# Kernel optimization log

Measured on AMD Instinct MI355X. Metric: run time of the kernel, lower is better.

The kernel has to match this reference:

```python
import jax, jax.numpy as jnp
import numpy as np

T = 4096
I = 512    # input_size
H = 2048   # hidden_layer_size
O = 1      # output_size

def setup_inputs() -> dict:
    key = jax.random.key(0)
    ks = jax.random.split(key, 7)
    s_ih = 1.0 / np.sqrt(H)
    return {
        "input_seq": jax.random.normal(ks[0], (T, I), dtype=jnp.float32),
        "W_ih": jax.random.uniform(ks[1], (4 * H, I), minval=-s_ih, maxval=s_ih, dtype=jnp.float32),
        "W_hh": jax.random.uniform(ks[2], (4 * H, H), minval=-s_ih, maxval=s_ih, dtype=jnp.float32),
        "b_ih": jax.random.uniform(ks[3], (4 * H,), minval=-s_ih, maxval=s_ih, dtype=jnp.float32),
        "b_hh": jax.random.uniform(ks[4], (4 * H,), minval=-s_ih, maxval=s_ih, dtype=jnp.float32),
        "W_lin": jax.random.uniform(ks[5], (O, H), minval=-s_ih, maxval=s_ih, dtype=jnp.float32),
        "b_lin": jax.random.uniform(ks[6], (O,), minval=-s_ih, maxval=s_ih, dtype=jnp.float32),
    }

def _lstm_last_h(x, W_ih, W_hh, b_ih, b_hh):
    # Precompute input contributions for all timesteps: [T, 4H]
    x_gates = x @ W_ih.T + (b_ih + b_hh)
    h0 = jnp.zeros((H,), dtype=x.dtype)
    c0 = jnp.zeros((H,), dtype=x.dtype)

    def step(carry, xg):
        h, c = carry
        gates = xg + h @ W_hh.T  # [4H]
        i, f, g, o = jnp.split(gates, 4)  # PyTorch gate order: i, f, g, o
        i = jax.nn.sigmoid(i)
        f = jax.nn.sigmoid(f)
        g = jnp.tanh(g)
        o = jax.nn.sigmoid(o)
        c = f * c + i * g
        h = o * jnp.tanh(c)
        return (h, c), None

    (h_T, _), _ = jax.lax.scan(step, (h0, c0), x_gates)
    return h_T

def reference(input_seq, W_ih, W_hh, b_ih, b_hh, W_lin, b_lin):
    # Module returns predictions[-1] = linear(lstm_out[-1]); only last h is needed.
    h_T = _lstm_last_h(input_seq, W_ih, W_hh, b_ih, b_hh)
    return h_T @ W_lin.T + b_lin  # shape [O]
```

## Files before the change

### kernel.cpp

```cpp
#include <hip/hip_runtime.h>


#define T_STEPS 4096
#define HID     2048
#define GATES   8192
#define KIN     512
#define NWG     256
#define NTHR    512
#define NREP    4
#define XG_BYTES ((size_t)T_STEPS * GATES * 4)
#define HCOM_BYTES ((size_t)NREP * 2 * HID * 8)

typedef float v2f __attribute__((ext_vector_type(2)));

__device__ __forceinline__ float u2f(unsigned int u) {
    union { unsigned int u; float f; } x; x.u = u; return x.f;
}
__device__ __forceinline__ float fast_sigmoid(float x) {
    return 1.f / (1.f + __expf(-x));
}
__device__ __forceinline__ float fast_tanh(float x) {
    return 2.f / (1.f + __expf(-2.f * x)) - 1.f;
}

__global__ __launch_bounds__(256) void gemm_xg(const float* __restrict__ A,
                                               const float* __restrict__ B,
                                               const float* __restrict__ bih,
                                               const float* __restrict__ bhh,
                                               float* __restrict__ C) {
    __shared__ float As[32][68];
    __shared__ float Bs[32][68];
    const int t  = threadIdx.x;
    const int tx = t & 15, ty = t >> 4;
    const int m0 = blockIdx.y * 64, n0 = blockIdx.x * 64;
    const int sr = t >> 3, sc = (t & 7) * 4;

    float c[4][4] = {};
    for (int k0 = 0; k0 < KIN; k0 += 32) {
        float4 a0 = *(const float4*)(A + (size_t)(m0 + sr)      * KIN + k0 + sc);
        float4 a1 = *(const float4*)(A + (size_t)(m0 + sr + 32) * KIN + k0 + sc);
        float4 b0 = *(const float4*)(B + (size_t)(n0 + sr)      * KIN + k0 + sc);
        float4 b1 = *(const float4*)(B + (size_t)(n0 + sr + 32) * KIN + k0 + sc);
        __syncthreads();
        As[sc+0][sr] = a0.x; As[sc+1][sr] = a0.y; As[sc+2][sr] = a0.z; As[sc+3][sr] = a0.w;
        As[sc+0][sr+32] = a1.x; As[sc+1][sr+32] = a1.y; As[sc+2][sr+32] = a1.z; As[sc+3][sr+32] = a1.w;
        Bs[sc+0][sr] = b0.x; Bs[sc+1][sr] = b0.y; Bs[sc+2][sr] = b0.z; Bs[sc+3][sr] = b0.w;
        Bs[sc+0][sr+32] = b1.x; Bs[sc+1][sr+32] = b1.y; Bs[sc+2][sr+32] = b1.z; Bs[sc+3][sr+32] = b1.w;
        __syncthreads();
#pragma unroll
        for (int kk = 0; kk < 32; ++kk) {
            float4 av = *(const float4*)&As[kk][ty * 4];
            float4 bv = *(const float4*)&Bs[kk][tx * 4];
            c[0][0] = fmaf(av.x, bv.x, c[0][0]); c[0][1] = fmaf(av.x, bv.y, c[0][1]);
            c[0][2] = fmaf(av.x, bv.z, c[0][2]); c[0][3] = fmaf(av.x, bv.w, c[0][3]);
            c[1][0] = fmaf(av.y, bv.x, c[1][0]); c[1][1] = fmaf(av.y, bv.y, c[1][1]);
            c[1][2] = fmaf(av.y, bv.z, c[1][2]); c[1][3] = fmaf(av.y, bv.w, c[1][3]);
            c[2][0] = fmaf(av.z, bv.x, c[2][0]); c[2][1] = fmaf(av.z, bv.y, c[2][1]);
            c[2][2] = fmaf(av.z, bv.z, c[2][2]); c[2][3] = fmaf(av.z, bv.w, c[2][3]);
            c[3][0] = fmaf(av.w, bv.x, c[3][0]); c[3][1] = fmaf(av.w, bv.y, c[3][1]);
            c[3][2] = fmaf(av.w, bv.z, c[3][2]); c[3][3] = fmaf(av.w, bv.w, c[3][3]);
        }
    }
    const int col = n0 + tx * 4;
    float4 bias;
    bias.x = bih[col]   + bhh[col];
    bias.y = bih[col+1] + bhh[col+1];
    bias.z = bih[col+2] + bhh[col+2];
    bias.w = bih[col+3] + bhh[col+3];
#pragma unroll
    for (int i = 0; i < 4; ++i) {
        float4 o;
        o.x = c[i][0] + bias.x; o.y = c[i][1] + bias.y;
        o.z = c[i][2] + bias.z; o.w = c[i][3] + bias.w;
        *(float4*)(C + (size_t)(m0 + ty * 4 + i) * GATES + col) = o;
    }
}

template<int USE_XG>
__global__ __launch_bounds__(NTHR, 2) void lstm_rec(
    const float* __restrict__ X,
    const float* __restrict__ Wih,
    const float* __restrict__ xg,
    const float* __restrict__ Whh,
    const float* __restrict__ bih,
    const float* __restrict__ bhh,
    unsigned long long* __restrict__ hcom)
{
    const int t  = threadIdx.x;
    const int kc = t & 127;
    const int rg = t >> 7;
    const int j0 = blockIdx.x * 8;
    const int rep = blockIdx.x & (NREP - 1);

    v2f whh2[8][8];
#pragma unroll
    for (int m = 0; m < 8; ++m) {
        const float* wr = Whh + (size_t)(rg * HID + j0 + m) * HID + kc;
#pragma unroll
        for (int j = 0; j < 8; ++j) {
            v2f p; p.x = wr[(2 * j) * 128]; p.y = wr[(2 * j + 1) * 128];
            whh2[m][j] = p;
        }
    }
    float wih[8][4];
    if (!USE_XG) {
#pragma unroll
        for (int m = 0; m < 8; ++m) {
            float4 vx = *(const float4*)(Wih + (size_t)(rg * HID + j0 + m) * KIN + kc * 4);
            wih[m][0] = vx.x; wih[m][1] = vx.y; wih[m][2] = vx.z; wih[m][3] = vx.w;
        }
    }

    float brow = 0.f;
    if (t < 32) {
        const int grow = (t >> 3) * HID + j0 + (t & 7);
        brow = bih[grow] + bhh[grow];
    }

    __shared__ float hshare[HID];
    __shared__ float part[32 * 132];
    float c_state = 0.f;

    for (int s = 0; s < T_STEPS; ++s) {
        float xgv = 0.f;
        if (USE_XG && t < 32)
            xgv = xg[(size_t)s * GATES + (t >> 3) * HID + j0 + (t & 7)];

        v2f hv2[8];
        if (t < 128) {
            if (t >= 64 && s > 0) __builtin_amdgcn_s_sleep(8);
            const unsigned long long* hp = hcom + ((size_t)rep * 2 + (s & 1)) * HID;
            unsigned long long v[16];
            int guard = 1 << 18;
            for (;;) {
#pragma unroll
                for (int g = 0; g < 16; ++g)
                    v[g] = __hip_atomic_load(hp + g * 128 + kc, __ATOMIC_RELAXED,
                                             __HIP_MEMORY_SCOPE_AGENT);
                bool ok = true;
#pragma unroll
                for (int g = 0; g < 16; ++g)
                    ok &= ((unsigned int)v[g] >= (unsigned int)s);
                if (ok || --guard <= 0) break;
                __builtin_amdgcn_s_sleep(1);
            }
#pragma unroll
            for (int j = 0; j < 8; ++j) {
                v2f p;
                p.x = u2f((unsigned int)(v[2 * j] >> 32));
                p.y = u2f((unsigned int)(v[2 * j + 1] >> 32));
                hv2[j] = p;
                hshare[(2 * j) * 128 + kc]     = p.x;
                hshare[(2 * j + 1) * 128 + kc] = p.y;
            }
        }
        __syncthreads();
        if (t >= 128) {
#pragma unroll
            for (int j = 0; j < 8; ++j) {
                v2f p;
                p.x = hshare[(2 * j) * 128 + kc];
                p.y = hshare[(2 * j + 1) * 128 + kc];
                hv2[j] = p;
            }
        }

        v2f acc2[8];
        if (!USE_XG) {
            float4 x4 = *(const float4*)(X + (size_t)s * KIN + kc * 4);
#pragma unroll
            for (int m = 0; m < 8; ++m) {
                float a = wih[m][0] * x4.x;
                a = fmaf(wih[m][1], x4.y, a);
                a = fmaf(wih[m][2], x4.z, a);
                a = fmaf(wih[m][3], x4.w, a);
                v2f z; z.x = a; z.y = 0.f; acc2[m] = z;
            }
        } else {
#pragma unroll
            for (int m = 0; m < 8; ++m) { v2f z; z.x = 0.f; z.y = 0.f; acc2[m] = z; }
        }

#pragma unroll
        for (int m = 0; m < 8; ++m) {
            v2f a = acc2[m];
#pragma unroll
            for (int j = 0; j < 8; ++j)
                a = __builtin_elementwise_fma(whh2[m][j], hv2[j], a);
            acc2[m] = a;
        }
#pragma unroll
        for (int m = 0; m < 8; ++m)
            part[(rg * 8 + m) * 132 + kc] = acc2[m].x + acc2[m].y;
        __syncthreads();

        if (t < 64) {
            const int row = t & 31, half = t >> 5;
            const float4* p4 = (const float4*)(part + row * 132 + half * 64);
            float s0 = 0.f, s1 = 0.f, s2 = 0.f, s3 = 0.f;
#pragma unroll
            for (int i = 0; i < 16; ++i) {
                float4 pv = p4[i];
                s0 += pv.x; s1 += pv.y; s2 += pv.z; s3 += pv.w;
            }
            float sum = (s0 + s1) + (s2 + s3);
            sum += __shfl_xor(sum, 32, 64);
            sum += brow + xgv;
            const float a1 = __shfl_down(sum, 8, 64);
            const float a2 = __shfl_down(sum, 16, 64);
            const float a3 = __shfl_down(sum, 24, 64);
            if (t < 8) {
                const float i_s = fast_sigmoid(sum);
                const float f_s = fast_sigmoid(a1);
                const float g_t = fast_tanh(a2);
                const float o_s = fast_sigmoid(a3);
                c_state = f_s * c_state + i_s * g_t;
                const float h = o_s * fast_tanh(c_state);
                const unsigned long long pk =
                    ((unsigned long long)__float_as_uint(h) << 32) | (unsigned int)(s + 1);
                const size_t slot = (size_t)((s + 1) & 1) * HID + j0 + t;
#pragma unroll
                for (int r = 0; r < NREP; ++r)
                    __hip_atomic_store(&hcom[(size_t)r * 2 * HID + slot], pk,
                                       __ATOMIC_RELAXED, __HIP_MEMORY_SCOPE_AGENT);
            }
        }
    }
}

__global__ __launch_bounds__(256) void final_linear(const unsigned long long* __restrict__ hcom,
                                                    const float* __restrict__ Wlin,
                                                    const float* __restrict__ blin,
                                                    float* __restrict__ out) {
    __shared__ float red[4];
    const int t = threadIdx.x;
    float a = 0.f;
#pragma unroll
    for (int e = 0; e < 8; ++e) {
        const int idx = t * 8 + e;
        a = fmaf(Wlin[idx], u2f((unsigned int)(hcom[idx] >> 32)), a);
    }
#pragma unroll
    for (int m = 1; m < 64; m <<= 1) a += __shfl_xor(a, m, 64);
    if ((t & 63) == 0) red[t >> 6] = a;
    __syncthreads();
    if (t == 0) out[0] = red[0] + red[1] + red[2] + red[3] + blin[0];
}

extern "C" void kernel_launch(void* const* d_in, const int* in_sizes, int n_in,
                              void* d_out, int out_size, void* d_ws, size_t ws_size,
                              hipStream_t stream) {
    const float* X    = (const float*)d_in[0];
    const float* Wih  = (const float*)d_in[1];
    const float* Whh  = (const float*)d_in[2];
    const float* bih  = (const float*)d_in[3];
    const float* bhh  = (const float*)d_in[4];
    const float* Wlin = (const float*)d_in[5];
    const float* blin = (const float*)d_in[6];
    float* out = (float*)d_out;

    char* ws = (char*)d_ws;
    const bool big = ws_size >= XG_BYTES + HCOM_BYTES;

    if (big) {
        float* xg = (float*)ws;
        unsigned long long* hcom = (unsigned long long*)(ws + XG_BYTES);
        (void)hipMemsetAsync(hcom, 0, HCOM_BYTES, stream);
        gemm_xg<<<dim3(GATES / 64, T_STEPS / 64), 256, 0, stream>>>(X, Wih, bih, bhh, xg);
        lstm_rec<1><<<dim3(NWG), dim3(NTHR), 0, stream>>>(X, Wih, xg, Whh, bih, bhh, hcom);
        final_linear<<<1, 256, 0, stream>>>(hcom, Wlin, blin, out);
    } else {
        unsigned long long* hcom = (unsigned long long*)ws;
        (void)hipMemsetAsync(hcom, 0, HCOM_BYTES, stream);
        lstm_rec<0><<<dim3(NWG), dim3(NTHR), 0, stream>>>(X, Wih, nullptr, Whh, bih, bhh, hcom);
        final_linear<<<1, 256, 0, stream>>>(hcom, Wlin, blin, out);
    }
}
```

Baseline: 10.54 ms.

## Restructure LSTM recurrence: one hidden unit per wave with shuffle reduction

Each of the 8 waves in a workgroup now owns one hidden unit and computes all four of its gates with a full-K dot product. The reduction uses wave shuffles, which removes the shared-memory partial-sum buffer and the second __syncthreads per step. The xg precompute layout is permuted so each workgroup reads its 32 gate values for a step contiguously. The number of h replicas is raised to 8, the spin loop polls two halves independently, and the sleep before reading h is shortened, all to cut the latency of the cross-workgroup handoff. In exchange, each wave spends more shuffle instructions per step, and the extra replicas add atomic stores.

```diff
diff --git a/kernel.cpp b/kernel.cpp
--- a/kernel.cpp
+++ b/kernel.cpp
@@ -7,7 +7,7 @@
 #define KIN     512
 #define NWG     256
 #define NTHR    512
-#define NREP    4
+#define NREP    8
 #define XG_BYTES ((size_t)T_STEPS * GATES * 4)
 #define HCOM_BYTES ((size_t)NREP * 2 * HID * 8)
 
@@ -67,12 +67,16 @@
     bias.y = bih[col+1] + bhh[col+1];
     bias.z = bih[col+2] + bhh[col+2];
     bias.w = bih[col+3] + bhh[col+3];
+    const int bb = (col >> 3) & (NWG - 1);
+    const int gg = col >> 11;
+    const int uu = col & 7;
+    float* dst = C + (size_t)bb * T_STEPS * 32 + gg * 8 + uu;
 #pragma unroll
     for (int i = 0; i < 4; ++i) {
         float4 o;
         o.x = c[i][0] + bias.x; o.y = c[i][1] + bias.y;
         o.z = c[i][2] + bias.z; o.w = c[i][3] + bias.w;
-        *(float4*)(C + (size_t)(m0 + ty * 4 + i) * GATES + col) = o;
+        *(float4*)(dst + (size_t)(m0 + ty * 4 + i) * 32) = o;
     }
 }
 
@@ -87,143 +91,155 @@
     unsigned long long* __restrict__ hcom)
 {
     const int t  = threadIdx.x;
-    const int kc = t & 127;
-    const int rg = t >> 7;
+    const int l  = t & 63;
+    const int w  = t >> 6;
     const int j0 = blockIdx.x * 8;
     const int rep = blockIdx.x & (NREP - 1);
 
-    v2f whh2[8][8];
-#pragma unroll
-    for (int m = 0; m < 8; ++m) {
-        const float* wr = Whh + (size_t)(rg * HID + j0 + m) * HID + kc;
-#pragma unroll
-        for (int j = 0; j < 8; ++j) {
-            v2f p; p.x = wr[(2 * j) * 128]; p.y = wr[(2 * j + 1) * 128];
-            whh2[m][j] = p;
-        }
-    }
-    float wih[8][4];
+    v2f whh2[4][16];
+#pragma unroll
+    for (int g = 0; g < 4; ++g) {
+        const float* wr = Whh + (size_t)(g * HID + j0 + w) * HID + 2 * l;
+#pragma unroll
+        for (int q = 0; q < 16; ++q)
+            whh2[g][q] = *(const v2f*)(wr + q * 128);
+    }
+
+    float wih[4][8];
     if (!USE_XG) {
 #pragma unroll
-        for (int m = 0; m < 8; ++m) {
-            float4 vx = *(const float4*)(Wih + (size_t)(rg * HID + j0 + m) * KIN + kc * 4);
-            wih[m][0] = vx.x; wih[m][1] = vx.y; wih[m][2] = vx.z; wih[m][3] = vx.w;
-        }
-    }
-
-    float brow = 0.f;
-    if (t < 32) {
-        const int grow = (t >> 3) * HID + j0 + (t & 7);
-        brow = bih[grow] + bhh[grow];
+        for (int g = 0; g < 4; ++g) {
+            const float* wr = Wih + (size_t)(g * HID + j0 + w) * KIN + l * 8;
+#pragma unroll
+            for (int e = 0; e < 8; ++e) wih[g][e] = wr[e];
+        }
+    }
+
+    float brow[4];
+#pragma unroll
+    for (int g = 0; g < 4; ++g) {
+        const int r = g * HID + j0 + w;
+        brow[g] = bih[r] + bhh[r];
     }
 
     __shared__ float hshare[HID];
-    __shared__ float part[32 * 132];
     float c_state = 0.f;
+    const int kc = t & 127;
+
+    unsigned long long va[8], vb[8];
 
     for (int s = 0; s < T_STEPS; ++s) {
-        float xgv = 0.f;
-        if (USE_XG && t < 32)
-            xgv = xg[(size_t)s * GATES + (t >> 3) * HID + j0 + (t & 7)];
-
-        v2f hv2[8];
+        float xgv[4] = {0.f, 0.f, 0.f, 0.f};
+        if (USE_XG) {
+            const float* xp = xg + ((size_t)blockIdx.x * T_STEPS + s) * 32 + w;
+#pragma unroll
+            for (int g = 0; g < 4; ++g) xgv[g] = xp[g * 8];
+        }
+        float xrow[4] = {0.f, 0.f, 0.f, 0.f};
+        if (!USE_XG) {
+            float4 x0 = *(const float4*)(X + (size_t)s * KIN + l * 8);
+            float4 x1 = *(const float4*)(X + (size_t)s * KIN + l * 8 + 4);
+#pragma unroll
+            for (int g = 0; g < 4; ++g) {
+                float a = wih[g][0] * x0.x;
+                a = fmaf(wih[g][1], x0.y, a);
+                a = fmaf(wih[g][2], x0.z, a);
+                a = fmaf(wih[g][3], x0.w, a);
+                a = fmaf(wih[g][4], x1.x, a);
+                a = fmaf(wih[g][5], x1.y, a);
+                a = fmaf(wih[g][6], x1.z, a);
+                a = fmaf(wih[g][7], x1.w, a);
+                xrow[g] = a;
+            }
+        }
+
         if (t < 128) {
-            if (t >= 64 && s > 0) __builtin_amdgcn_s_sleep(8);
+            if (t >= 64 && s > 0) __builtin_amdgcn_s_sleep(2);
             const unsigned long long* hp = hcom + ((size_t)rep * 2 + (s & 1)) * HID;
-            unsigned long long v[16];
+#pragma unroll
+            for (int m = 0; m < 8; ++m)
+                va[m] = __hip_atomic_load(hp + m * 128 + kc, __ATOMIC_RELAXED,
+                                          __HIP_MEMORY_SCOPE_AGENT);
+#pragma unroll
+            for (int m = 0; m < 8; ++m)
+                vb[m] = __hip_atomic_load(hp + (m + 8) * 128 + kc, __ATOMIC_RELAXED,
+                                          __HIP_MEMORY_SCOPE_AGENT);
+            bool okA = false, okB = false;
             int guard = 1 << 18;
             for (;;) {
-#pragma unroll
-                for (int g = 0; g < 16; ++g)
-                    v[g] = __hip_atomic_load(hp + g * 128 + kc, __ATOMIC_RELAXED,
-                                             __HIP_MEMORY_SCOPE_AGENT);
-                bool ok = true;
-#pragma unroll
-                for (int g = 0; g < 16; ++g)
-                    ok &= ((unsigned int)v[g] >= (unsigned int)s);
-                if (ok || --guard <= 0) break;
-                __builtin_amdgcn_s_sleep(1);
+                if (!okA) {
+                    bool ok = true;
+#pragma unroll
+                    for (int m = 0; m < 8; ++m)
+                        ok &= ((unsigned int)va[m] >= (unsigned int)s);
+                    okA = ok;
+                    if (!okA) {
+#pragma unroll
+                        for (int m = 0; m < 8; ++m)
+                            va[m] = __hip_atomic_load(hp + m * 128 + kc, __ATOMIC_RELAXED,
+                                                      __HIP_MEMORY_SCOPE_AGENT);
+                    }
+                }
+                if (okA && okB) break;
+                if (!okB) {
+                    if (!okA) __builtin_amdgcn_s_sleep(6);
+                    bool ok = true;
+#pragma unroll
+                    for (int m = 0; m < 8; ++m)
+                        ok &= ((unsigned int)vb[m] >= (unsigned int)s);
+                    okB = ok;
+                    if (!okB) {
+#pragma unroll
+                        for (int m = 0; m < 8; ++m)
+                            vb[m] = __hip_atomic_load(hp + (m + 8) * 128 + kc, __ATOMIC_RELAXED,
+                                                      __HIP_MEMORY_SCOPE_AGENT);
+                    }
+                }
+                if (okA && okB) break;
+                if (--guard <= 0) break;
             }
 #pragma unroll
-            for (int j = 0; j < 8; ++j) {
-                v2f p;
-                p.x = u2f((unsigned int)(v[2 * j] >> 32));
-                p.y = u2f((unsigned int)(v[2 * j + 1] >> 32));
-                hv2[j] = p;
-                hshare[(2 * j) * 128 + kc]     = p.x;
-                hshare[(2 * j + 1) * 128 + kc] = p.y;
+            for (int m = 0; m < 8; ++m) {
+                hshare[m * 128 + kc]       = u2f((unsigned int)(va[m] >> 32));
+                hshare[(m + 8) * 128 + kc] = u2f((unsigned int)(vb[m] >> 32));
             }
         }
         __syncthreads();
-        if (t >= 128) {
-#pragma unroll
-            for (int j = 0; j < 8; ++j) {
-                v2f p;
-                p.x = hshare[(2 * j) * 128 + kc];
-                p.y = hshare[(2 * j + 1) * 128 + kc];
-                hv2[j] = p;
-            }
-        }
-
-        v2f acc2[8];
-        if (!USE_XG) {
-            float4 x4 = *(const float4*)(X + (size_t)s * KIN + kc * 4);
-#pragma unroll
-            for (int m = 0; m < 8; ++m) {
-                float a = wih[m][0] * x4.x;
-                a = fmaf(wih[m][1], x4.y, a);
-                a = fmaf(wih[m][2], x4.z, a);
-                a = fmaf(wih[m][3], x4.w, a);
-                v2f z; z.x = a; z.y = 0.f; acc2[m] = z;
-            }
-        } else {
-#pragma unroll
-            for (int m = 0; m < 8; ++m) { v2f z; z.x = 0.f; z.y = 0.f; acc2[m] = z; }
-        }
-
-#pragma unroll
-        for (int m = 0; m < 8; ++m) {
-            v2f a = acc2[m];
-#pragma unroll
-            for (int j = 0; j < 8; ++j)
-                a = __builtin_elementwise_fma(whh2[m][j], hv2[j], a);
-            acc2[m] = a;
-        }
-#pragma unroll
-        for (int m = 0; m < 8; ++m)
-            part[(rg * 8 + m) * 132 + kc] = acc2[m].x + acc2[m].y;
-        __syncthreads();
-
-        if (t < 64) {
-            const int row = t & 31, half = t >> 5;
-            const float4* p4 = (const float4*)(part + row * 132 + half * 64);
-            float s0 = 0.f, s1 = 0.f, s2 = 0.f, s3 = 0.f;
-#pragma unroll
-            for (int i = 0; i < 16; ++i) {
-                float4 pv = p4[i];
-                s0 += pv.x; s1 += pv.y; s2 += pv.z; s3 += pv.w;
-            }
-            float sum = (s0 + s1) + (s2 + s3);
-            sum += __shfl_xor(sum, 32, 64);
-            sum += brow + xgv;
-            const float a1 = __shfl_down(sum, 8, 64);
-            const float a2 = __shfl_down(sum, 16, 64);
-            const float a3 = __shfl_down(sum, 24, 64);
-            if (t < 8) {
-                const float i_s = fast_sigmoid(sum);
-                const float f_s = fast_sigmoid(a1);
-                const float g_t = fast_tanh(a2);
-                const float o_s = fast_sigmoid(a3);
-                c_state = f_s * c_state + i_s * g_t;
-                const float h = o_s * fast_tanh(c_state);
-                const unsigned long long pk =
-                    ((unsigned long long)__float_as_uint(h) << 32) | (unsigned int)(s + 1);
-                const size_t slot = (size_t)((s + 1) & 1) * HID + j0 + t;
-#pragma unroll
-                for (int r = 0; r < NREP; ++r)
-                    __hip_atomic_store(&hcom[(size_t)r * 2 * HID + slot], pk,
-                                       __ATOMIC_RELAXED, __HIP_MEMORY_SCOPE_AGENT);
-            }
+
+        v2f hv2[16];
+#pragma unroll
+        for (int q = 0; q < 16; ++q)
+            hv2[q] = *(const v2f*)&hshare[2 * l + 128 * q];
+
+        float sg[4];
+#pragma unroll
+        for (int g = 0; g < 4; ++g) {
+            v2f a; a.x = xrow[g]; a.y = 0.f;
+#pragma unroll
+            for (int q = 0; q < 16; ++q)
+                a = __builtin_elementwise_fma(whh2[g][q], hv2[q], a);
+            sg[g] = a.x + a.y;
+        }
+#pragma unroll
+        for (int m = 1; m < 64; m <<= 1) {
+#pragma unroll
+            for (int g = 0; g < 4; ++g)
+                sg[g] += __shfl_xor(sg[g], m, 64);
+        }
+
+        const float i_s = fast_sigmoid(sg[0] + brow[0] + xgv[0]);
+        const float f_s = fast_sigmoid(sg[1] + brow[1] + xgv[1]);
+        const float g_t = fast_tanh   (sg[2] + brow[2] + xgv[2]);
+        const float o_s = fast_sigmoid(sg[3] + brow[3] + xgv[3]);
+        c_state = f_s * c_state + i_s * g_t;
+        const float h = o_s * fast_tanh(c_state);
+
+        if (l < NREP) {
+            const unsigned long long pk =
+                ((unsigned long long)__float_as_uint(h) << 32) | (unsigned int)(s + 1);
+            __hip_atomic_store(hcom + (size_t)l * 2 * HID +
+                                   (size_t)((s + 1) & 1) * HID + j0 + w,
+                               pk, __ATOMIC_RELAXED, __HIP_MEMORY_SCOPE_AGENT);
         }
     }
 }
```

Result: slower. 20.33 ms (+92.9%).
